# Performance work log

Hardware: AMD Instinct MI355X
Metric: run time of the kernel (lower is better)

Reference implementation:

```python
import jax, jax.numpy as jnp
import numpy as np

B, H, W = 4, 64, 64
INPLANES, PLANES, G, K = 608, 152, 19, 3
KK = K * K
EPS = 1e-5


def conv2d(x, w, stride=1, padding=0, dilation=1):
    return jax.lax.conv_general_dilated(
        x, w, (stride, stride), [(padding, padding)] * 2,
        rhs_dilation=(dilation, dilation),
        dimension_numbers=("NCHW", "OIHW", "NCHW"))


def bn(x, g, b, m, v):
    # inference-mode batchnorm (affine with running stats)
    inv = g / jnp.sqrt(v + EPS)
    return x * inv[None, :, None, None] + (b - m * inv)[None, :, None, None]


def deform_conv(x, offset, w, pad=1, dil=1):
    # x: [B,C,H,W], offset: [B, 2*G*KK, H, W] ((dy,dx) pairs per group per tap), w: [Cout,C,K,K]
    Bs, C, Hh, Ww = x.shape
    Cg = C // G
    off = offset.reshape(Bs, G, KK, 2, Hh, Ww)
    ky, kx = jnp.meshgrid(jnp.arange(K), jnp.arange(K), indexing="ij")
    base_y = (jnp.arange(Hh) - pad)[None, None, None, :, None] + (dil * ky.reshape(-1))[None, None, :, None, None]
    base_x = (jnp.arange(Ww) - pad)[None, None, None, None, :] + (dil * kx.reshape(-1))[None, None, :, None, None]
    ys = base_y + off[:, :, :, 0]  # [B,G,KK,H,W]
    xs = base_x + off[:, :, :, 1]
    y0 = jnp.floor(ys)
    x0 = jnp.floor(xs)
    wy = ys - y0
    wx = xs - x0
    y0i = y0.astype(jnp.int32)
    x0i = x0.astype(jnp.int32)
    xf = x.reshape(Bs, G, Cg, Hh * Ww)

    def gather(yi, xi, wgt):
        valid = ((yi >= 0) & (yi < Hh) & (xi >= 0) & (xi < Ww)).astype(x.dtype)
        idx = jnp.clip(yi, 0, Hh - 1) * Ww + jnp.clip(xi, 0, Ww - 1)
        idxf = jnp.broadcast_to(idx.reshape(Bs, G, 1, KK * Hh * Ww), (Bs, G, Cg, KK * Hh * Ww))
        g = jnp.take_along_axis(xf, idxf, axis=3).reshape(Bs, G, Cg, KK, Hh, Ww)
        return g * (wgt * valid)[:, :, None]

    samp = (gather(y0i, x0i, (1 - wy) * (1 - wx))
            + gather(y0i, x0i + 1, (1 - wy) * wx)
            + gather(y0i + 1, x0i, wy * (1 - wx))
            + gather(y0i + 1, x0i + 1, wy * wx))  # [B,G,Cg,KK,H,W]
    wr = w.reshape(w.shape[0], G, Cg, KK)
    return jnp.einsum("bgckhw,ogck->bohw", samp, wr)


def setup_inputs() -> dict:
    key = jax.random.key(0)
    ks = jax.random.split(key, 8)
    d = {}
    d["x"] = jax.random.normal(ks[0], (B, INPLANES, H, W), jnp.float32)
    d["conv1_w"] = jax.random.normal(ks[1], (PLANES, INPLANES, 1, 1), jnp.float32) * 0.05
    d["conv2_w"] = jax.random.normal(ks[2], (2 * G * KK, PLANES, 3, 3), jnp.float32) * 0.01
    d["dconv_w"] = jax.random.normal(ks[3], (PLANES, PLANES, 3, 3), jnp.float32) * 0.05
    d["conv3_w"] = jax.random.normal(ks[4], (4 * PLANES, PLANES, 1, 1), jnp.float32) * 0.05
    for i, (name, c) in enumerate([("bn1", PLANES), ("bn2", PLANES), ("bn3", 4 * PLANES)]):
        k1, k2, k3, k4 = jax.random.split(ks[5 + i], 4)
        d[name + "_g"] = jax.random.uniform(k1, (c,), jnp.float32, 0.5, 1.5)
        d[name + "_b"] = jax.random.normal(k2, (c,), jnp.float32) * 0.1
        d[name + "_m"] = jax.random.normal(k3, (c,), jnp.float32) * 0.1
        d[name + "_v"] = jax.random.uniform(k4, (c,), jnp.float32, 0.5, 1.5)
    return d


def reference(x, conv1_w, conv2_w, dconv_w, conv3_w,
              bn1_g, bn1_b, bn1_m, bn1_v,
              bn2_g, bn2_b, bn2_m, bn2_v,
              bn3_g, bn3_b, bn3_m, bn3_v):
    out = jax.nn.relu(conv2d(x, conv1_w))           # conv1 -> relu (order as in source)
    out = bn(out, bn1_g, bn1_b, bn1_m, bn1_v)       # -> bn1
    offset = conv2d(out, conv2_w, padding=1)         # offset-generating 3x3 conv
    out = deform_conv(out, offset, dconv_w)          # deformable 3x3 conv
    out = bn(jax.nn.relu(out), bn2_g, bn2_b, bn2_m, bn2_v)
    out = bn(conv2d(out, conv3_w), bn3_g, bn3_b, bn3_m, bn3_v)
    return jax.nn.relu(out + x)
```

## Files before the change

### kernel.cpp

```cpp
#include <hip/hip_runtime.h>

#define EPSV 1e-5f

typedef __bf16 bf16_t;
typedef __bf16 bf16x8 __attribute__((ext_vector_type(8)));
typedef float f32x4 __attribute__((ext_vector_type(4)));

__device__ inline bf16x8 bzero8() {
  bf16x8 z;
#pragma unroll
  for (int i = 0; i < 8; i++) z[i] = (bf16_t)0.f;
  return z;
}

__device__ inline f32x4 mfma16(bf16x8 a, bf16x8 b, f32x4 c) {
  return __builtin_amdgcn_mfma_f32_16x16x32_bf16(a, b, c, 0, 0, 0);
}

#define W1E (160 * 608)
#define W2E (384 * 1376)
#define WDE (192 * 1376)
#define W3E (640 * 160)

__global__ __launch_bounds__(256) void prep_weights(
    const float* __restrict__ w1, const float* __restrict__ w2,
    const float* __restrict__ wd, const float* __restrict__ w3,
    bf16_t* __restrict__ w1b, bf16_t* __restrict__ w2b,
    bf16_t* __restrict__ wdb, bf16_t* __restrict__ w3b) {
  int i = blockIdx.x * 256 + threadIdx.x;
  float v = 0.f;
  if (i < W1E) {
    int oc = i / 608, ic = i % 608;
    if (oc < 152) v = w1[oc * 608 + ic];
    w1b[i] = (bf16_t)v;
  } else if (i < W1E + W2E) {
    int j = i - W1E;
    int oc = j / 1376, k = j % 1376;
    if (oc < 342 && k < 1368) {
      int t = k / 152, ic = k % 152;
      v = w2[(oc * 152 + ic) * 9 + t];
    }
    w2b[j] = (bf16_t)v;
  } else if (i < W1E + W2E + WDE) {
    int j = i - W1E - W2E;
    int o = j / 1376, k = j % 1376;
    if (o < 152 && k < 1368) {
      int t = k / 152, ic = k % 152;
      v = wd[(o * 152 + ic) * 9 + t];
    }
    wdb[j] = (bf16_t)v;
  } else if (i < W1E + W2E + WDE + W3E) {
    int j = i - W1E - W2E - WDE;
    int oc = j / 160, ic = j % 160;
    if (oc < 608 && ic < 152) v = w3[oc * 152 + ic];
    w3b[j] = (bf16_t)v;
  }
}

__global__ void prep_bn(const float* g1, const float* b1, const float* m1, const float* v1,
                        const float* g2, const float* b2, const float* m2, const float* v2,
                        const float* g3, const float* b3, const float* m3, const float* v3,
                        float* __restrict__ bnc) {
  int i = threadIdx.x;
  if (i < 152) {
    float inv = g1[i] / sqrtf(v1[i] + EPSV);
    bnc[i] = inv;
    bnc[152 + i] = b1[i] - m1[i] * inv;
    float inv2 = g2[i] / sqrtf(v2[i] + EPSV);
    bnc[304 + i] = inv2;
    bnc[456 + i] = b2[i] - m2[i] * inv2;
  }
  if (i < 608) {
    float inv3 = g3[i] / sqrtf(v3[i] + EPSV);
    bnc[608 + i] = inv3;
    bnc[1216 + i] = b3[i] - m3[i] * inv3;
  }
}

__global__ __launch_bounds__(256) void s1_conv1(const float* __restrict__ x,
                                                const bf16_t* __restrict__ w1b,
                                                const float* __restrict__ bnc,
                                                bf16_t* __restrict__ out1) {
  __shared__ bf16_t t1[32 * 616];
  int tid = threadIdx.x;
  int px0 = blockIdx.x * 32;
  int b = px0 >> 12, sp0 = px0 & 4095;
  for (int task = tid; task < 608 * 8; task += 256) {
    int c = task >> 3, i4 = task & 7;
    f32x4 v = *(const f32x4*)(x + (((size_t)(b * 608 + c)) << 12) + sp0 + i4 * 4);
#pragma unroll
    for (int i = 0; i < 4; i++) t1[(i4 * 4 + i) * 616 + c] = (bf16_t)v[i];
  }
  __syncthreads();
  int wid = tid >> 6, lane = tid & 63, q = lane >> 4, lr = lane & 15;
  int mw = wid & 1, nw = wid >> 1;
  f32x4 acc[5];
#pragma unroll
  for (int n = 0; n < 5; n++) acc[n] = (f32x4){0.f, 0.f, 0.f, 0.f};
  for (int kk = 0; kk < 19; kk++) {
    int k0 = kk * 32 + q * 8;
    bf16x8 a = *(const bf16x8*)(t1 + (mw * 16 + lr) * 616 + k0);
#pragma unroll
    for (int n = 0; n < 5; n++) {
      bf16x8 bf = *(const bf16x8*)(w1b + (nw * 80 + n * 16 + lr) * 608 + k0);
      acc[n] = mfma16(a, bf, acc[n]);
    }
  }
#pragma unroll
  for (int n = 0; n < 5; n++) {
    int oc = nw * 80 + n * 16 + lr;
    if (oc < 152) {
      float inv = bnc[oc], beta = bnc[152 + oc];
#pragma unroll
      for (int i = 0; i < 4; i++) {
        int p = px0 + mw * 16 + q * 4 + i;
        float v = fmaxf(acc[n][i], 0.f) * inv + beta;
        out1[(size_t)p * 152 + oc] = (bf16_t)v;
      }
    }
  }
}

__global__ __launch_bounds__(512) void s2_offs(const bf16_t* __restrict__ out1,
                                               const bf16_t* __restrict__ w2b,
                                               float* __restrict__ offs) {
  __shared__ bf16_t t2[102 * 152];
  int tid = threadIdx.x;
  int xh = blockIdx.x & 1, y = (blockIdx.x >> 1) & 63, b = blockIdx.x >> 7;
  const bf16_t* ob = out1 + (((size_t)b) << 12) * 152;
  int x0 = xh * 32 - 1;
  for (int task = tid; task < 3 * 34 * 19; task += 512) {
    int j = task / 646, r = task % 646;
    int xi = r / 19, cb = r % 19;
    int yy = y + j - 1, xx = x0 + xi;
    bf16x8 v = bzero8();
    if (yy >= 0 && yy < 64 && xx >= 0 && xx < 64)
      v = *(const bf16x8*)(ob + (size_t)(yy * 64 + xx) * 152 + cb * 8);
    *(bf16x8*)(t2 + (j * 34 + xi) * 152 + cb * 8) = v;
  }
  __syncthreads();
  int wid = tid >> 6, lane = tid & 63, q = lane >> 4, lr = lane & 15;
  f32x4 acc[2][3];
#pragma unroll
  for (int m = 0; m < 2; m++)
#pragma unroll
    for (int n = 0; n < 3; n++) acc[m][n] = (f32x4){0.f, 0.f, 0.f, 0.f};
  for (int kk = 0; kk < 43; kk++) {
    int k0 = kk * 32 + q * 8;
    bf16x8 a[2];
    if (k0 < 1368) {
      int t = k0 / 152, c0 = k0 - t * 152;
      int dy = t / 3, dxp1 = t - dy * 3;
      int base = (dy * 34 + lr + dxp1) * 152 + c0;
#pragma unroll
      for (int m = 0; m < 2; m++) a[m] = *(const bf16x8*)(t2 + base + m * 16 * 152);
    } else {
      a[0] = bzero8();
      a[1] = bzero8();
    }
#pragma unroll
    for (int n = 0; n < 3; n++) {
      bf16x8 bf = *(const bf16x8*)(w2b + (size_t)(wid * 48 + n * 16 + lr) * 1376 + k0);
#pragma unroll
      for (int m = 0; m < 2; m++) acc[m][n] = mfma16(a[m], bf, acc[m][n]);
    }
  }
#pragma unroll
  for (int n = 0; n < 3; n++) {
    int col = wid * 48 + n * 16 + lr;
    if (col < 342) {
      int g = col / 18, rem = col % 18;
      int t = rem >> 1, c = rem & 1;
      int pos = t * 38 + g * 2 + c;
#pragma unroll
      for (int m = 0; m < 2; m++)
#pragma unroll
        for (int i = 0; i < 4; i++) {
          int p = (b << 12) + y * 64 + xh * 32 + m * 16 + q * 4 + i;
          offs[(size_t)p * 344 + pos] = acc[m][n][i];
        }
    }
  }
}

__global__ __launch_bounds__(256, 3) void s3_dconv(const bf16_t* __restrict__ out1,
                                                   const float* __restrict__ offs,
                                                   const bf16_t* __restrict__ wdb,
                                                   const float* __restrict__ bnc,
                                                   bf16_t* __restrict__ a2) {
  __shared__ bf16_t alds[16 * 1368];
  int tid = threadIdx.x;
  int row0 = blockIdx.x * 16;
  if (tid < 171) {
    int t = tid / 19, g = tid - t * 19;
    int ky = t / 3, kx = t - ky * 3;
    int bb = row0 >> 12;
    const bf16_t* base = out1 + (((size_t)bb << 12) * 152) + g * 8;
    const float* op0 = offs + (size_t)row0 * 344 + t * 38 + g * 2;
    bf16_t* ldst = alds + t * 152 + g * 8;
#pragma unroll
    for (int r = 0; r < 16; r++) {
      int p = row0 + r;
      int y = (p >> 6) & 63, xc = p & 63;
      float2 ov = *(const float2*)(op0 + (size_t)r * 344);
      float ys = (float)(y - 1 + ky) + ov.x;
      float xs = (float)(xc - 1 + kx) + ov.y;
      float y0f = floorf(ys), x0f = floorf(xs);
      float wy = ys - y0f, wx = xs - x0f;
      int y0 = (int)y0f, x0 = (int)x0f;
      float fa[8];
#pragma unroll
      for (int i = 0; i < 8; i++) fa[i] = 0.f;
      float wws[4] = {(1.f - wy) * (1.f - wx), (1.f - wy) * wx,
                      wy * (1.f - wx), wy * wx};
      int yy[4] = {y0, y0, y0 + 1, y0 + 1};
      int xx[4] = {x0, x0 + 1, x0, x0 + 1};
#pragma unroll
      for (int cn = 0; cn < 4; cn++) {
        if (yy[cn] >= 0 && yy[cn] < 64 && xx[cn] >= 0 && xx[cn] < 64) {
          bf16x8 v = *(const bf16x8*)(base + (size_t)(yy[cn] * 64 + xx[cn]) * 152);
#pragma unroll
          for (int i = 0; i < 8; i++) fa[i] += wws[cn] * (float)v[i];
        }
      }
      bf16x8 o;
#pragma unroll
      for (int i = 0; i < 8; i++) o[i] = (bf16_t)fa[i];
      *(bf16x8*)(ldst + r * 1368) = o;
    }
  }
  __syncthreads();
  int wid = tid >> 6, lane = tid & 63, q = lane >> 4, lr = lane & 15;
  int nb = wid * 3;
  f32x4 acc[3];
#pragma unroll
  for (int n = 0; n < 3; n++) acc[n] = (f32x4){0.f, 0.f, 0.f, 0.f};
  for (int kk = 0; kk < 43; kk++) {
    int k0 = kk * 32 + q * 8;
    bf16x8 a = (k0 < 1368) ? *(const bf16x8*)(alds + lr * 1368 + k0) : bzero8();
#pragma unroll
    for (int n = 0; n < 3; n++) {
      bf16x8 bf = *(const bf16x8*)(wdb + (size_t)((nb + n) * 16 + lr) * 1376 + k0);
      acc[n] = mfma16(a, bf, acc[n]);
    }
  }
#pragma unroll
  for (int n = 0; n < 3; n++) {
    int oc = (nb + n) * 16 + lr;
    if (oc < 152) {
      float inv = bnc[304 + oc], beta = bnc[456 + oc];
#pragma unroll
      for (int i = 0; i < 4; i++) {
        int p = row0 + q * 4 + i;
        float v = fmaxf(acc[n][i], 0.f) * inv + beta;
        a2[(size_t)p * 152 + oc] = (bf16_t)v;
      }
    }
  }
}

__global__ __launch_bounds__(256) void s4_conv3(const bf16_t* __restrict__ a2,
                                                const bf16_t* __restrict__ w3b,
                                                const float* __restrict__ bnc,
                                                const float* __restrict__ x,
                                                float* __restrict__ out) {
  int tid = threadIdx.x;
  int wid = tid >> 6, lane = tid & 63, q = lane >> 4, lr = lane & 15;
  int p0 = blockIdx.x * 16;
  int b = p0 >> 12, sp0 = p0 & 4095;
  f32x4 acc[10];
#pragma unroll
  for (int n = 0; n < 10; n++) acc[n] = (f32x4){0.f, 0.f, 0.f, 0.f};
  for (int kk = 0; kk < 5; kk++) {
    int k0 = kk * 32 + q * 8;
    bf16x8 a = (k0 < 152) ? *(const bf16x8*)(a2 + (size_t)(p0 + lr) * 152 + k0) : bzero8();
#pragma unroll
    for (int n = 0; n < 10; n++) {
      bf16x8 bf = *(const bf16x8*)(w3b + (size_t)(wid * 160 + n * 16 + lr) * 160 + k0);
      acc[n] = mfma16(a, bf, acc[n]);
    }
  }
#pragma unroll
  for (int n = 0; n < 10; n++) {
    int oc = wid * 160 + n * 16 + lr;
    if (oc < 608) {
      float inv = bnc[608 + oc], beta = bnc[1216 + oc];
      size_t gi = (((size_t)(b * 608 + oc)) << 12) + sp0 + q * 4;
      f32x4 xr = *(const f32x4*)(x + gi);
      f32x4 o;
#pragma unroll
      for (int i = 0; i < 4; i++) o[i] = fmaxf(acc[n][i] * inv + beta + xr[i], 0.f);
      *(f32x4*)(out + gi) = o;
    }
  }
}

extern "C" void kernel_launch(void* const* d_in, const int* in_sizes, int n_in,
                              void* d_out, int out_size, void* d_ws, size_t ws_size,
                              hipStream_t stream) {
  const float* x = (const float*)d_in[0];
  const float* w1 = (const float*)d_in[1];
  const float* w2 = (const float*)d_in[2];
  const float* wd = (const float*)d_in[3];
  const float* w3 = (const float*)d_in[4];
  const float* g1 = (const float*)d_in[5];
  const float* b1 = (const float*)d_in[6];
  const float* m1 = (const float*)d_in[7];
  const float* v1 = (const float*)d_in[8];
  const float* g2 = (const float*)d_in[9];
  const float* b2 = (const float*)d_in[10];
  const float* m2 = (const float*)d_in[11];
  const float* v2 = (const float*)d_in[12];
  const float* g3 = (const float*)d_in[13];
  const float* b3 = (const float*)d_in[14];
  const float* m3 = (const float*)d_in[15];
  const float* v3 = (const float*)d_in[16];

  char* ws = (char*)d_ws;
  bf16_t* w1b = (bf16_t*)(ws + 0);
  bf16_t* w2b = (bf16_t*)(ws + 194560);
  bf16_t* wdb = (bf16_t*)(ws + 1251328);
  bf16_t* w3b = (bf16_t*)(ws + 1779712);
  float* bnc = (float*)(ws + 1984512);
  bf16_t* out1 = (bf16_t*)(ws + 1991808);
  float* offs = (float*)(ws + 6972544);
  bf16_t* a2 = (bf16_t*)(ws + 29516928);
  float* out = (float*)d_out;

  prep_weights<<<3876, 256, 0, stream>>>(w1, w2, wd, w3, w1b, w2b, wdb, w3b);
  prep_bn<<<1, 640, 0, stream>>>(g1, b1, m1, v1, g2, b2, m2, v2, g3, b3, m3, v3, bnc);
  s1_conv1<<<512, 256, 0, stream>>>(x, w1b, bnc, out1);
  s2_offs<<<512, 512, 0, stream>>>(out1, w2b, offs);
  s3_dconv<<<1024, 256, 0, stream>>>(out1, offs, wdb, bnc, a2);
  s4_conv3<<<1024, 256, 0, stream>>>(a2, w3b, bnc, x, out);
}
```

Before: 202.7 us.

## Pipeline deformable sampling per tap with double-buffered LDS and MFMA

```diff
diff --git a/kernel.cpp b/kernel.cpp
--- a/kernel.cpp
+++ b/kernel.cpp
@@ -19,7 +19,7 @@
 
 #define W1E (160 * 608)
 #define W2E (384 * 1376)
-#define WDE (192 * 1376)
+#define WDE (192 * 1440)
 #define W3E (640 * 160)
 
 __global__ __launch_bounds__(256) void prep_weights(
@@ -43,11 +43,9 @@
     w2b[j] = (bf16_t)v;
   } else if (i < W1E + W2E + WDE) {
     int j = i - W1E - W2E;
-    int o = j / 1376, k = j % 1376;
-    if (o < 152 && k < 1368) {
-      int t = k / 152, ic = k % 152;
-      v = wd[(o * 152 + ic) * 9 + t];
-    }
+    int o = j / 1440, k = j % 1440;
+    int t = k / 160, ic = k % 160;
+    if (o < 152 && ic < 152) v = wd[(o * 152 + ic) * 9 + t];
     wdb[j] = (bf16_t)v;
   } else if (i < W1E + W2E + WDE + W3E) {
     int j = i - W1E - W2E - WDE;
@@ -183,70 +181,95 @@
   }
 }
 
-__global__ __launch_bounds__(256, 3) void s3_dconv(const bf16_t* __restrict__ out1,
+__global__ __launch_bounds__(256, 4) void s3_dconv(const bf16_t* __restrict__ out1,
                                                    const float* __restrict__ offs,
                                                    const bf16_t* __restrict__ wdb,
                                                    const float* __restrict__ bnc,
                                                    bf16_t* __restrict__ a2) {
-  __shared__ bf16_t alds[16 * 1368];
+  __shared__ float olds[16 * 344];
+  __shared__ bf16_t abuf[2 * 16 * 168];
   int tid = threadIdx.x;
   int row0 = blockIdx.x * 16;
-  if (tid < 171) {
-    int t = tid / 19, g = tid - t * 19;
-    int ky = t / 3, kx = t - ky * 3;
-    int bb = row0 >> 12;
-    const bf16_t* base = out1 + (((size_t)bb << 12) * 152) + g * 8;
-    const float* op0 = offs + (size_t)row0 * 344 + t * 38 + g * 2;
-    bf16_t* ldst = alds + t * 152 + g * 8;
-#pragma unroll
-    for (int r = 0; r < 16; r++) {
-      int p = row0 + r;
-      int y = (p >> 6) & 63, xc = p & 63;
-      float2 ov = *(const float2*)(op0 + (size_t)r * 344);
-      float ys = (float)(y - 1 + ky) + ov.x;
-      float xs = (float)(xc - 1 + kx) + ov.y;
-      float y0f = floorf(ys), x0f = floorf(xs);
-      float wy = ys - y0f, wx = xs - x0f;
-      int y0 = (int)y0f, x0 = (int)x0f;
-      float fa[8];
-#pragma unroll
-      for (int i = 0; i < 8; i++) fa[i] = 0.f;
-      float wws[4] = {(1.f - wy) * (1.f - wx), (1.f - wy) * wx,
-                      wy * (1.f - wx), wy * wx};
-      int yy[4] = {y0, y0, y0 + 1, y0 + 1};
-      int xx[4] = {x0, x0 + 1, x0, x0 + 1};
-#pragma unroll
-      for (int cn = 0; cn < 4; cn++) {
-        if (yy[cn] >= 0 && yy[cn] < 64 && xx[cn] >= 0 && xx[cn] < 64) {
-          bf16x8 v = *(const bf16x8*)(base + (size_t)(yy[cn] * 64 + xx[cn]) * 152);
-#pragma unroll
-          for (int i = 0; i < 8; i++) fa[i] += wws[cn] * (float)v[i];
-        }
+  int bb = row0 >> 12;
+  const bf16_t* obase = out1 + (((size_t)bb << 12) * 152);
+  if (tid < 64) {
+    int cur = tid >> 5, r = (tid >> 1) & 15, ch = tid & 1;
+    *(bf16x8*)(abuf + cur * 2688 + r * 168 + 152 + ch * 8) = bzero8();
+  }
+  for (int task = tid; task < 16 * 86; task += 256) {
+    int r = task / 86, cc = task - r * 86;
+    *(f32x4*)(olds + r * 344 + cc * 4) =
+        *(const f32x4*)(offs + (size_t)(row0 + r) * 344 + cc * 4);
+  }
+  __syncthreads();
+
+  int wid = tid >> 6, lane = tid & 63, q = lane >> 4, lr = lane & 15;
+  f32x4 acc[3];
+#pragma unroll
+  for (int n = 0; n < 3; n++) acc[n] = (f32x4){0.f, 0.f, 0.f, 0.f};
+
+#define SAMPLE_TAP(T, CUR)                                                        \
+  {                                                                               \
+    int t_ = (T);                                                                 \
+    int ky = t_ / 3, kx = t_ - ky * 3;                                            \
+    for (int task = tid; task < 304; task += 256) {                               \
+      int r = task / 19, g = task - r * 19;                                       \
+      int p = row0 + r;                                                           \
+      int y = (p >> 6) & 63, xc = p & 63;                                         \
+      float2 ov = *(const float2*)(olds + r * 344 + t_ * 38 + g * 2);             \
+      float ys = (float)(y - 1 + ky) + ov.x;                                      \
+      float xs = (float)(xc - 1 + kx) + ov.y;                                     \
+      float y0f = floorf(ys), x0f = floorf(xs);                                   \
+      float wy = ys - y0f, wx = xs - x0f;                                         \
+      int y0 = (int)y0f, x0 = (int)x0f;                                           \
+      int y1 = y0 + 1, x1 = x0 + 1;                                               \
+      int y0c = min(max(y0, 0), 63), x0c = min(max(x0, 0), 63);                   \
+      int y1c = min(max(y1, 0), 63), x1c = min(max(x1, 0), 63);                   \
+      float vy0 = (y0 == y0c) ? 1.f : 0.f;                                        \
+      float vy1 = (y1 == y1c) ? 1.f : 0.f;                                        \
+      float vx0 = (x0 == x0c) ? 1.f : 0.f;                                        \
+      float vx1 = (x1 == x1c) ? 1.f : 0.f;                                        \
+      float w00 = (1.f - wy) * (1.f - wx) * vy0 * vx0;                            \
+      float w01 = (1.f - wy) * wx * vy0 * vx1;                                    \
+      float w10 = wy * (1.f - wx) * vy1 * vx0;                                    \
+      float w11 = wy * wx * vy1 * vx1;                                            \
+      const bf16_t* bg = obase + g * 8;                                           \
+      bf16x8 c00 = *(const bf16x8*)(bg + (size_t)(y0c * 64 + x0c) * 152);         \
+      bf16x8 c01 = *(const bf16x8*)(bg + (size_t)(y0c * 64 + x1c) * 152);         \
+      bf16x8 c10 = *(const bf16x8*)(bg + (size_t)(y1c * 64 + x0c) * 152);         \
+      bf16x8 c11 = *(const bf16x8*)(bg + (size_t)(y1c * 64 + x1c) * 152);         \
+      bf16x8 o;                                                                   \
+      _Pragma("unroll") for (int i = 0; i < 8; i++) {                             \
+        float f = w00 * (float)c00[i];                                            \
+        f = fmaf(w01, (float)c01[i], f);                                          \
+        f = fmaf(w10, (float)c10[i], f);                                          \
+        f = fmaf(w11, (float)c11[i], f);                                          \
+        o[i] = (bf16_t)f;                                                         \
+      }                                                                           \
+      *(bf16x8*)(abuf + (CUR)*2688 + r * 168 + g * 8) = o;                        \
+    }                                                                             \
+  }
+
+  SAMPLE_TAP(0, 0)
+  __syncthreads();
+  for (int t = 0; t < 9; t++) {
+    int cur = t & 1;
+    if (t < 8) SAMPLE_TAP(t + 1, cur ^ 1)
+#pragma unroll
+    for (int kk = 0; kk < 5; kk++) {
+      int k0 = kk * 32 + q * 8;
+      bf16x8 a = *(const bf16x8*)(abuf + cur * 2688 + lr * 168 + k0);
+#pragma unroll
+      for (int n = 0; n < 3; n++) {
+        bf16x8 bf = *(const bf16x8*)(wdb + (size_t)((wid * 3 + n) * 16 + lr) * 1440 + t * 160 + k0);
+        acc[n] = mfma16(a, bf, acc[n]);
       }
-      bf16x8 o;
-#pragma unroll
-      for (int i = 0; i < 8; i++) o[i] = (bf16_t)fa[i];
-      *(bf16x8*)(ldst + r * 1368) = o;
-    }
-  }
-  __syncthreads();
-  int wid = tid >> 6, lane = tid & 63, q = lane >> 4, lr = lane & 15;
-  int nb = wid * 3;
-  f32x4 acc[3];
-#pragma unroll
-  for (int n = 0; n < 3; n++) acc[n] = (f32x4){0.f, 0.f, 0.f, 0.f};
-  for (int kk = 0; kk < 43; kk++) {
-    int k0 = kk * 32 + q * 8;
-    bf16x8 a = (k0 < 1368) ? *(const bf16x8*)(alds + lr * 1368 + k0) : bzero8();
-#pragma unroll
-    for (int n = 0; n < 3; n++) {
-      bf16x8 bf = *(const bf16x8*)(wdb + (size_t)((nb + n) * 16 + lr) * 1376 + k0);
-      acc[n] = mfma16(a, bf, acc[n]);
-    }
+    }
+    __syncthreads();
   }
 #pragma unroll
   for (int n = 0; n < 3; n++) {
-    int oc = (nb + n) * 16 + lr;
+    int oc = (wid * 3 + n) * 16 + lr;
     if (oc < 152) {
       float inv = bnc[304 + oc], beta = bnc[456 + oc];
 #pragma unroll
@@ -257,6 +280,7 @@
       }
     }
   }
+#undef SAMPLE_TAP
 }
 
 __global__ __launch_bounds__(256) void s4_conv3(const bf16_t* __restrict__ a2,
@@ -320,14 +344,14 @@
   bf16_t* w1b = (bf16_t*)(ws + 0);
   bf16_t* w2b = (bf16_t*)(ws + 194560);
   bf16_t* wdb = (bf16_t*)(ws + 1251328);
-  bf16_t* w3b = (bf16_t*)(ws + 1779712);
-  float* bnc = (float*)(ws + 1984512);
-  bf16_t* out1 = (bf16_t*)(ws + 1991808);
-  float* offs = (float*)(ws + 6972544);
-  bf16_t* a2 = (bf16_t*)(ws + 29516928);
+  bf16_t* w3b = (bf16_t*)(ws + 1804288);
+  float* bnc = (float*)(ws + 2009088);
+  bf16_t* out1 = (bf16_t*)(ws + 2016384);
+  float* offs = (float*)(ws + 6997120);
+  bf16_t* a2 = (bf16_t*)(ws + 29541504);
   float* out = (float*)d_out;
 
-  prep_weights<<<3876, 256, 0, stream>>>(w1, w2, wd, w3, w1b, w2b, wdb, w3b);
+  prep_weights<<<3924, 256, 0, stream>>>(w1, w2, wd, w3, w1b, w2b, wdb, w3b);
   prep_bn<<<1, 640, 0, stream>>>(g1, b1, m1, v1, g2, b2, m2, v2, g3, b3, m3, v3, bnc);
   s1_conv1<<<512, 256, 0, stream>>>(x, w1b, bnc, out1);
   s2_offs<<<512, 512, 0, stream>>>(out1, w2b, offs);
```

Result: faster. 176.7 us (-12.8%).

## Split deformable conv into a parallel sampling kernel and a separate GEMM kernel

Applied to the files above, without the earlier changes.

```diff
diff --git a/kernel.cpp b/kernel.cpp
--- a/kernel.cpp
+++ b/kernel.cpp
@@ -121,137 +121,149 @@
   }
 }
 
-__global__ __launch_bounds__(512) void s2_offs(const bf16_t* __restrict__ out1,
-                                               const bf16_t* __restrict__ w2b,
-                                               float* __restrict__ offs) {
-  __shared__ bf16_t t2[102 * 152];
+__global__ __launch_bounds__(256, 4) void s2_offs(const bf16_t* __restrict__ out1,
+                                                  const bf16_t* __restrict__ w2b,
+                                                  float* __restrict__ offs) {
+  __shared__ bf16_t t2[3 * 34 * 156];
   int tid = threadIdx.x;
-  int xh = blockIdx.x & 1, y = (blockIdx.x >> 1) & 63, b = blockIdx.x >> 7;
+  int nh = blockIdx.x & 1;
+  int rest = blockIdx.x >> 1;
+  int xh = rest & 1, y = (rest >> 1) & 63, b = rest >> 7;
   const bf16_t* ob = out1 + (((size_t)b) << 12) * 152;
   int x0 = xh * 32 - 1;
-  for (int task = tid; task < 3 * 34 * 19; task += 512) {
+  for (int task = tid; task < 3 * 34 * 19; task += 256) {
     int j = task / 646, r = task % 646;
     int xi = r / 19, cb = r % 19;
     int yy = y + j - 1, xx = x0 + xi;
     bf16x8 v = bzero8();
     if (yy >= 0 && yy < 64 && xx >= 0 && xx < 64)
       v = *(const bf16x8*)(ob + (size_t)(yy * 64 + xx) * 152 + cb * 8);
-    *(bf16x8*)(t2 + (j * 34 + xi) * 152 + cb * 8) = v;
+    *(bf16x8*)(t2 + (j * 34 + xi) * 156 + cb * 8) = v;
   }
   __syncthreads();
   int wid = tid >> 6, lane = tid & 63, q = lane >> 4, lr = lane & 15;
+  int ncol0 = nh * 192 + wid * 48;
   f32x4 acc[2][3];
 #pragma unroll
   for (int m = 0; m < 2; m++)
 #pragma unroll
     for (int n = 0; n < 3; n++) acc[m][n] = (f32x4){0.f, 0.f, 0.f, 0.f};
+  const bf16_t* wb = w2b + (size_t)(ncol0 + lr) * 1376;
+#pragma unroll
   for (int kk = 0; kk < 43; kk++) {
     int k0 = kk * 32 + q * 8;
+    bf16x8 bfr[3];
+#pragma unroll
+    for (int n = 0; n < 3; n++)
+      bfr[n] = *(const bf16x8*)(wb + (size_t)(n * 16) * 1376 + k0);
     bf16x8 a[2];
     if (k0 < 1368) {
       int t = k0 / 152, c0 = k0 - t * 152;
       int dy = t / 3, dxp1 = t - dy * 3;
-      int base = (dy * 34 + lr + dxp1) * 152 + c0;
-#pragma unroll
-      for (int m = 0; m < 2; m++) a[m] = *(const bf16x8*)(t2 + base + m * 16 * 152);
+#pragma unroll
+      for (int m = 0; m < 2; m++)
+        a[m] = *(const bf16x8*)(t2 + (dy * 34 + m * 16 + lr + dxp1) * 156 + c0);
     } else {
       a[0] = bzero8();
       a[1] = bzero8();
     }
 #pragma unroll
-    for (int n = 0; n < 3; n++) {
-      bf16x8 bf = *(const bf16x8*)(w2b + (size_t)(wid * 48 + n * 16 + lr) * 1376 + k0);
-#pragma unroll
-      for (int m = 0; m < 2; m++) acc[m][n] = mfma16(a[m], bf, acc[m][n]);
-    }
+    for (int n = 0; n < 3; n++)
+#pragma unroll
+      for (int m = 0; m < 2; m++) acc[m][n] = mfma16(a[m], bfr[n], acc[m][n]);
   }
 #pragma unroll
   for (int n = 0; n < 3; n++) {
-    int col = wid * 48 + n * 16 + lr;
+    int col = ncol0 + n * 16 + lr;
     if (col < 342) {
-      int g = col / 18, rem = col % 18;
-      int t = rem >> 1, c = rem & 1;
-      int pos = t * 38 + g * 2 + c;
 #pragma unroll
       for (int m = 0; m < 2; m++)
 #pragma unroll
         for (int i = 0; i < 4; i++) {
           int p = (b << 12) + y * 64 + xh * 32 + m * 16 + q * 4 + i;
-          offs[(size_t)p * 344 + pos] = acc[m][n][i];
+          offs[(size_t)p * 344 + col] = acc[m][n][i];
         }
     }
   }
 }
 
-__global__ __launch_bounds__(256, 3) void s3_dconv(const bf16_t* __restrict__ out1,
-                                                   const float* __restrict__ offs,
+__global__ __launch_bounds__(256, 8) void s3a_sample(const bf16_t* __restrict__ out1,
+                                                     const float* __restrict__ offs,
+                                                     bf16_t* __restrict__ samp,
+                                                     int p_base) {
+  int task = blockIdx.x * 256 + threadIdx.x;
+  int lp = task / 171, s = task - lp * 171;
+  int t = s / 19, g = s - t * 19;
+  int p = p_base + lp;
+  int b = p >> 12, y = (p >> 6) & 63, xc = p & 63;
+  int ky = t / 3, kx = t - ky * 3;
+  float2 ov = *(const float2*)(offs + (size_t)p * 344 + g * 18 + t * 2);
+  float ys = (float)(y - 1 + ky) + ov.x;
+  float xs = (float)(xc - 1 + kx) + ov.y;
+  float y0f = floorf(ys), x0f = floorf(xs);
+  float wy = ys - y0f, wx = xs - x0f;
+  int y0 = (int)y0f, x0 = (int)x0f;
+  int y1 = y0 + 1, x1 = x0 + 1;
+  int y0c = min(max(y0, 0), 63), x0c = min(max(x0, 0), 63);
+  int y1c = min(max(y1, 0), 63), x1c = min(max(x1, 0), 63);
+  float vy0 = (y0 == y0c) ? 1.f : 0.f;
+  float vy1 = (y1 == y1c) ? 1.f : 0.f;
+  float vx0 = (x0 == x0c) ? 1.f : 0.f;
+  float vx1 = (x1 == x1c) ? 1.f : 0.f;
+  float w00 = (1.f - wy) * (1.f - wx) * vy0 * vx0;
+  float w01 = (1.f - wy) * wx * vy0 * vx1;
+  float w10 = wy * (1.f - wx) * vy1 * vx0;
+  float w11 = wy * wx * vy1 * vx1;
+  const bf16_t* bg = out1 + (((size_t)b << 12) * 152) + g * 8;
+  bf16x8 c00 = *(const bf16x8*)(bg + (size_t)(y0c * 64 + x0c) * 152);
+  bf16x8 c01 = *(const bf16x8*)(bg + (size_t)(y0c * 64 + x1c) * 152);
+  bf16x8 c10 = *(const bf16x8*)(bg + (size_t)(y1c * 64 + x0c) * 152);
+  bf16x8 c11 = *(const bf16x8*)(bg + (size_t)(y1c * 64 + x1c) * 152);
+  bf16x8 o;
+#pragma unroll
+  for (int i = 0; i < 8; i++) {
+    float f = w00 * (float)c00[i];
+    f = fmaf(w01, (float)c01[i], f);
+    f = fmaf(w10, (float)c10[i], f);
+    f = fmaf(w11, (float)c11[i], f);
+    o[i] = (bf16_t)f;
+  }
+  *(bf16x8*)(samp + (size_t)lp * 1376 + t * 152 + g * 8) = o;
+  if (s == 170) *(bf16x8*)(samp + (size_t)lp * 1376 + 1368) = bzero8();
+}
+
+__global__ __launch_bounds__(512, 4) void s3b_gemm(const bf16_t* __restrict__ samp,
                                                    const bf16_t* __restrict__ wdb,
                                                    const float* __restrict__ bnc,
-                                                   bf16_t* __restrict__ a2) {
-  __shared__ bf16_t alds[16 * 1368];
+                                                   bf16_t* __restrict__ a2,
+                                                   int p_base) {
   int tid = threadIdx.x;
-  int row0 = blockIdx.x * 16;
-  if (tid < 171) {
-    int t = tid / 19, g = tid - t * 19;
-    int ky = t / 3, kx = t - ky * 3;
-    int bb = row0 >> 12;
-    const bf16_t* base = out1 + (((size_t)bb << 12) * 152) + g * 8;
-    const float* op0 = offs + (size_t)row0 * 344 + t * 38 + g * 2;
-    bf16_t* ldst = alds + t * 152 + g * 8;
-#pragma unroll
-    for (int r = 0; r < 16; r++) {
-      int p = row0 + r;
-      int y = (p >> 6) & 63, xc = p & 63;
-      float2 ov = *(const float2*)(op0 + (size_t)r * 344);
-      float ys = (float)(y - 1 + ky) + ov.x;
-      float xs = (float)(xc - 1 + kx) + ov.y;
-      float y0f = floorf(ys), x0f = floorf(xs);
-      float wy = ys - y0f, wx = xs - x0f;
-      int y0 = (int)y0f, x0 = (int)x0f;
-      float fa[8];
-#pragma unroll
-      for (int i = 0; i < 8; i++) fa[i] = 0.f;
-      float wws[4] = {(1.f - wy) * (1.f - wx), (1.f - wy) * wx,
-                      wy * (1.f - wx), wy * wx};
-      int yy[4] = {y0, y0, y0 + 1, y0 + 1};
-      int xx[4] = {x0, x0 + 1, x0, x0 + 1};
-#pragma unroll
-      for (int cn = 0; cn < 4; cn++) {
-        if (yy[cn] >= 0 && yy[cn] < 64 && xx[cn] >= 0 && xx[cn] < 64) {
-          bf16x8 v = *(const bf16x8*)(base + (size_t)(yy[cn] * 64 + xx[cn]) * 152);
-#pragma unroll
-          for (int i = 0; i < 8; i++) fa[i] += wws[cn] * (float)v[i];
-        }
-      }
-      bf16x8 o;
-#pragma unroll
-      for (int i = 0; i < 8; i++) o[i] = (bf16_t)fa[i];
-      *(bf16x8*)(ldst + r * 1368) = o;
-    }
-  }
-  __syncthreads();
   int wid = tid >> 6, lane = tid & 63, q = lane >> 4, lr = lane & 15;
-  int nb = wid * 3;
+  int mw = wid & 1, nw = wid >> 1;
+  int lrow = blockIdx.x * 32 + mw * 16;
+  const bf16_t* arow = samp + (size_t)(lrow + lr) * 1376;
+  const bf16_t* wb = wdb + (size_t)(nw * 48 + lr) * 1376;
   f32x4 acc[3];
 #pragma unroll
   for (int n = 0; n < 3; n++) acc[n] = (f32x4){0.f, 0.f, 0.f, 0.f};
+#pragma unroll
   for (int kk = 0; kk < 43; kk++) {
     int k0 = kk * 32 + q * 8;
-    bf16x8 a = (k0 < 1368) ? *(const bf16x8*)(alds + lr * 1368 + k0) : bzero8();
+    bf16x8 a = *(const bf16x8*)(arow + k0);
 #pragma unroll
     for (int n = 0; n < 3; n++) {
-      bf16x8 bf = *(const bf16x8*)(wdb + (size_t)((nb + n) * 16 + lr) * 1376 + k0);
+      bf16x8 bf = *(const bf16x8*)(wb + (size_t)(n * 16) * 1376 + k0);
       acc[n] = mfma16(a, bf, acc[n]);
     }
   }
 #pragma unroll
   for (int n = 0; n < 3; n++) {
-    int oc = (nb + n) * 16 + lr;
+    int oc = nw * 48 + n * 16 + lr;
     if (oc < 152) {
       float inv = bnc[304 + oc], beta = bnc[456 + oc];
 #pragma unroll
       for (int i = 0; i < 4; i++) {
-        int p = row0 + q * 4 + i;
+        int p = p_base + lrow + q * 4 + i;
         float v = fmaxf(acc[n][i], 0.f) * inv + beta;
         a2[(size_t)p * 152 + oc] = (bf16_t)v;
       }
@@ -325,12 +337,23 @@
   bf16_t* out1 = (bf16_t*)(ws + 1991808);
   float* offs = (float*)(ws + 6972544);
   bf16_t* a2 = (bf16_t*)(ws + 29516928);
+  bf16_t* samp = (bf16_t*)(ws + 34497664);
   float* out = (float*)d_out;
 
   prep_weights<<<3876, 256, 0, stream>>>(w1, w2, wd, w3, w1b, w2b, wdb, w3b);
   prep_bn<<<1, 640, 0, stream>>>(g1, b1, m1, v1, g2, b2, m2, v2, g3, b3, m3, v3, bnc);
   s1_conv1<<<512, 256, 0, stream>>>(x, w1b, bnc, out1);
-  s2_offs<<<512, 512, 0, stream>>>(out1, w2b, offs);
-  s3_dconv<<<1024, 256, 0, stream>>>(out1, offs, wdb, bnc, a2);
+  s2_offs<<<1024, 256, 0, stream>>>(out1, w2b, offs);
+
+  size_t base = 34497664;
+  int nchunk = 1;
+  if (ws_size < base + (size_t)16384 * 1376 * 2) nchunk = 4;
+  if (nchunk == 4 && ws_size < base + (size_t)4096 * 1376 * 2) nchunk = 16;
+  int npix = 16384 / nchunk;
+  for (int c = 0; c < nchunk; c++) {
+    s3a_sample<<<npix * 171 / 256, 256, 0, stream>>>(out1, offs, samp, c * npix);
+    s3b_gemm<<<npix / 32, 512, 0, stream>>>(samp, wdb, bnc, a2, c * npix);
+  }
+
   s4_conv3<<<1024, 256, 0, stream>>>(a2, w3b, bnc, x, out);
 }
```

Measured after the change: 182.4 us. -10.0%, faster.
